# Kernel tuning notes

Measured on AMD Instinct MI355X. Metric: run time of the kernel, lower is better.

The kernel has to match this reference:

```python
import jax, jax.numpy as jnp
import numpy as np

D = 512      # input_size
BR = 4       # branching factor (fan-in per internal node)
DEPTH = 8    # leaf level index; levels 0..DEPTH, root at level 0
N_NODES = (BR ** (DEPTH + 1) - 1) // (BR - 1)  # 87381


def setup_inputs() -> dict:
    key = jax.random.key(0)
    k1, k2, k3 = jax.random.split(key, 3)
    vectors = jax.random.normal(k1, (N_NODES, D), dtype=jnp.float32)
    scale = 1.0 / np.sqrt(D)
    wl = jax.random.normal(k2, (D, D), dtype=jnp.float32) * scale
    wr = jax.random.normal(k3, (D, D), dtype=jnp.float32) * scale
    return {"vectors": vectors, "wl": wl, "wr": wr, "branching": BR, "depth": DEPTH}


def reference(vectors, wl, wr, branching, depth):
    """Levelized CBTree forward over a complete `branching`-ary tree.

    vectors: [N, D] BFS-ordered node vectors (level l starts at (B^l-1)/(B-1)).
    Per node: h = tanh(x + sum_i lc_i * (h_i @ wl.T) + rc_i * (h_i @ wr.T)).
    """
    B, L = int(branching), int(depth)
    d = vectors.shape[-1]
    if B > 1:
        ind = jnp.arange(1, B + 1, dtype=vectors.dtype)  # 1-based child index
        lc = (B - ind) / (B - 1)
        rc = (ind - 1) / (B - 1)
    else:
        lc = jnp.full((1,), 0.5, dtype=vectors.dtype)
        rc = lc
    offsets = [(B ** l - 1) // (B - 1) for l in range(L + 1)]
    # leaves contribute their raw vectors (child.vector, no transform at leaf)
    h = vectors[offsets[L]: offsets[L] + B ** L]
    for l in range(L - 1, -1, -1):
        n = B ** l
        x = vectors[offsets[l]: offsets[l] + n]          # [n, D]
        hc = h.reshape(n, B, d)                           # children of level l
        tl = jnp.einsum('nbd,ed->nbe', hc, wl)            # wl(h_i) (Linear: h @ W.T)
        tr = jnp.einsum('nbd,ed->nbe', hc, wr)
        agg = jnp.einsum('b,nbe->ne', lc, tl) + jnp.einsum('b,nbe->ne', rc, tr)
        h = jnp.tanh(x + agg)                             # [n, D]
    return h  # [1, D] root hidden state
```

## Files before the change

kernel.cpp:

```cpp
#include <hip/hip_runtime.h>

typedef short short8 __attribute__((ext_vector_type(8)));
typedef float f32x4 __attribute__((ext_vector_type(4)));

#define D 512
#define KDIM 1024

static __device__ __forceinline__ unsigned short f2b(float f) {
    unsigned u = __builtin_bit_cast(unsigned, f);
    unsigned r = (u + 0x7fffu + ((u >> 16) & 1u)) >> 16;
    return (unsigned short)r;
}
static __device__ __forceinline__ float b2f(unsigned short u) {
    return __builtin_bit_cast(float, ((unsigned)u) << 16);
}
static __device__ __forceinline__ void split(float v, unsigned short& hi, unsigned short& lo) {
    hi = f2b(v);
    lo = f2b(v - b2f(hi));
}

static __device__ __forceinline__ void g2lds(const void* g, void* l) {
    __builtin_amdgcn_global_load_lds(
        (const __attribute__((address_space(1))) unsigned int*)g,
        (__attribute__((address_space(3))) unsigned int*)l, 16, 0, 0);
}

__global__ void pre_kernel(const float* __restrict__ leaves,
                           const float* __restrict__ wl, const float* __restrict__ wr,
                           unsigned short* __restrict__ Ah7,
                           unsigned short* __restrict__ Wh, unsigned short* __restrict__ Wl,
                           unsigned short* __restrict__ zbase) {
    int b = blockIdx.x;
    if (b < 4096) {
        int t = b * 256 + threadIdx.x;
        int p = t >> 6;
        int kc = (t & 63) << 3;
        const float c13 = 1.0f / 3.0f, c23 = 2.0f / 3.0f;
        const float* child = leaves;
        float4 a0 = *reinterpret_cast<const float4*>(child + (size_t)(4 * p + 0) * D + kc);
        float4 a1 = *reinterpret_cast<const float4*>(child + (size_t)(4 * p + 0) * D + kc + 4);
        float4 b0 = *reinterpret_cast<const float4*>(child + (size_t)(4 * p + 1) * D + kc);
        float4 b1 = *reinterpret_cast<const float4*>(child + (size_t)(4 * p + 1) * D + kc + 4);
        float4 c0 = *reinterpret_cast<const float4*>(child + (size_t)(4 * p + 2) * D + kc);
        float4 c1 = *reinterpret_cast<const float4*>(child + (size_t)(4 * p + 2) * D + kc + 4);
        float4 d0 = *reinterpret_cast<const float4*>(child + (size_t)(4 * p + 3) * D + kc);
        float4 d1 = *reinterpret_cast<const float4*>(child + (size_t)(4 * p + 3) * D + kc + 4);
        float ca[8] = {a0.x, a0.y, a0.z, a0.w, a1.x, a1.y, a1.z, a1.w};
        float cb[8] = {b0.x, b0.y, b0.z, b0.w, b1.x, b1.y, b1.z, b1.w};
        float cc[8] = {c0.x, c0.y, c0.z, c0.w, c1.x, c1.y, c1.z, c1.w};
        float cd[8] = {d0.x, d0.y, d0.z, d0.w, d1.x, d1.y, d1.z, d1.w};
        short8 uh, vh;
#pragma unroll
        for (int j = 0; j < 8; ++j) {
            float u = ca[j] + c23 * cb[j] + c13 * cc[j];
            float v = c13 * cb[j] + c23 * cc[j] + cd[j];
            uh[j] = (short)f2b(u);
            vh[j] = (short)f2b(v);
        }
        *reinterpret_cast<short8*>(&Ah7[(size_t)p * KDIM + kc]) = uh;
        *reinterpret_cast<short8*>(&Ah7[(size_t)p * KDIM + 512 + kc]) = vh;
    } else if (b < 6144) {
        int t = (b - 4096) * 256 + threadIdx.x;
        int e = t >> 10, k = t & 1023;
        float v = (k < 512) ? wl[e * 512 + k] : wr[e * 512 + (k - 512)];
        unsigned short h, l;
        split(v, h, l);
        Wh[t] = h; Wl[t] = l;
    } else {
        int t = (b - 6144) * 256 + threadIdx.x;
        *reinterpret_cast<short8*>(zbase + (size_t)t * 8) = (short8)0;
    }
}

template <int BM, bool ALO, bool WLO>
__global__ __launch_bounds__(256)
void gemm_tanh(const unsigned short* __restrict__ Ah, const unsigned short* __restrict__ Al,
               const unsigned short* __restrict__ Wh, const unsigned short* __restrict__ Wl,
               const float* __restrict__ x,
               unsigned short* __restrict__ nAh, unsigned short* __restrict__ nAl,
               int n) {
    constexpr int MF = (BM == 128) ? 4 : 2;
    constexpr int NF = 4;
    constexpr int APASS = BM / 32;
    __shared__ __align__(16) unsigned short Ahs[BM][64];
    __shared__ __align__(16) unsigned short Als[ALO ? BM : 1][64];
    __shared__ __align__(16) unsigned short Bhs[128][64];
    __shared__ __align__(16) unsigned short Bls[WLO ? 128 : 1][64];
    const int m0 = blockIdx.x * BM;
    const int e0 = blockIdx.y * 128;
    const int tid = threadIdx.x;
    const int lane = tid & 63, wid = tid >> 6;
    const int wr = (wid >> 1) * (BM / 2);
    const int wc = (wid & 1) * 64;

    f32x4 acc[MF][NF];
#pragma unroll
    for (int m = 0; m < MF; ++m)
#pragma unroll
        for (int nn = 0; nn < NF; ++nn) acc[m][nn] = (f32x4){0.f, 0.f, 0.f, 0.f};

    const int lrow = lane >> 3;
    const int lcol = (lane & 7) << 3;

    for (int kb = 0; kb < KDIM; kb += 64) {
#pragma unroll
        for (int p = 0; p < APASS; ++p) {
            int row = p * 32 + wid * 8;
            size_t g = (size_t)(m0 + row + lrow) * KDIM + kb + lcol;
            g2lds(&Ah[g], &Ahs[row][0]);
            if (ALO) g2lds(&Al[g], &Als[ALO ? row : 0][0]);
        }
#pragma unroll
        for (int p = 0; p < 4; ++p) {
            int row = p * 32 + wid * 8;
            size_t g = (size_t)(e0 + row + lrow) * KDIM + kb + lcol;
            g2lds(&Wh[g], &Bhs[row][0]);
            if (WLO) g2lds(&Wl[g], &Bls[WLO ? row : 0][0]);
        }
        __syncthreads();
#pragma unroll
        for (int kk = 0; kk < 64; kk += 32) {
            const int ka = kk + ((lane >> 4) << 3);
            short8 afh[MF], afl[MF], bfh[NF], bfl[NF];
#pragma unroll
            for (int m = 0; m < MF; ++m) {
                afh[m] = *reinterpret_cast<const short8*>(&Ahs[wr + m * 16 + (lane & 15)][ka]);
                if (ALO) afl[m] = *reinterpret_cast<const short8*>(&Als[ALO ? (wr + m * 16 + (lane & 15)) : 0][ka]);
            }
#pragma unroll
            for (int nn = 0; nn < NF; ++nn) {
                bfh[nn] = *reinterpret_cast<const short8*>(&Bhs[wc + nn * 16 + (lane & 15)][ka]);
                if (WLO) bfl[nn] = *reinterpret_cast<const short8*>(&Bls[WLO ? (wc + nn * 16 + (lane & 15)) : 0][ka]);
            }
#pragma unroll
            for (int m = 0; m < MF; ++m)
#pragma unroll
                for (int nn = 0; nn < NF; ++nn) {
                    acc[m][nn] = __builtin_amdgcn_mfma_f32_16x16x32_bf16(afh[m], bfh[nn], acc[m][nn], 0, 0, 0);
                    if (WLO)
                        acc[m][nn] = __builtin_amdgcn_mfma_f32_16x16x32_bf16(afh[m], bfl[nn], acc[m][nn], 0, 0, 0);
                    if (ALO)
                        acc[m][nn] = __builtin_amdgcn_mfma_f32_16x16x32_bf16(afl[m], bfh[nn], acc[m][nn], 0, 0, 0);
                }
        }
        __syncthreads();
    }

    const int dr = (lane >> 4) << 2;
    const int dc = lane & 15;
    const float c13 = 1.0f / 3.0f, c23 = 2.0f / 3.0f;
#pragma unroll
    for (int m = 0; m < MF; ++m) {
        int rbase = m0 + wr + m * 16 + dr;
        if (rbase >= n) continue;
#pragma unroll
        for (int nn = 0; nn < NF; ++nn) {
            int col = e0 + wc + nn * 16 + dc;
            float hv[4];
#pragma unroll
            for (int j = 0; j < 4; ++j) {
                int row = rbase + j;
                hv[j] = (row < n) ? tanhf(acc[m][nn][j] + x[(size_t)row * D + col]) : 0.f;
            }
            int p = rbase >> 2;
            float u = hv[0] + c23 * hv[1] + c13 * hv[2];
            float v = c13 * hv[1] + c23 * hv[2] + hv[3];
            unsigned short h_, l_;
            split(u, h_, l_);
            nAh[(size_t)p * KDIM + col] = h_;
            nAl[(size_t)p * KDIM + col] = l_;
            split(v, h_, l_);
            nAh[(size_t)p * KDIM + 512 + col] = h_;
            nAl[(size_t)p * KDIM + 512 + col] = l_;
        }
    }
}

#define TBUF 6
template <bool FINAL>
__global__ __launch_bounds__(256)
void gemm_tiny(const unsigned short* __restrict__ Ah, const unsigned short* __restrict__ Al,
               const unsigned short* __restrict__ Wh, const unsigned short* __restrict__ Wl,
               const float* __restrict__ x,
               unsigned short* __restrict__ nAh, unsigned short* __restrict__ nAl,
               float* __restrict__ out, int n) {
    __shared__ __align__(16) unsigned short AhS[TBUF][32][64];
    __shared__ __align__(16) unsigned short AlS[TBUF][32][64];
    __shared__ __align__(16) unsigned short BhS[TBUF][64][64];
    __shared__ __align__(16) unsigned short BlS[TBUF][64][64];
    const int m0 = blockIdx.x * 32;
    const int e0 = blockIdx.y * 64;
    const int tid = threadIdx.x;
    const int lane = tid & 63, wid = tid >> 6;
    const int lrow = lane >> 3, lcol = (lane & 7) << 3;

    auto stage = [&](int s) {
        int slot = s % TBUF;
        int kb = s * 64;
        {
            int row = wid * 8;
            size_t g = (size_t)(m0 + row + lrow) * KDIM + kb + lcol;
            g2lds(&Ah[g], &AhS[slot][row][0]);
            g2lds(&Al[g], &AlS[slot][row][0]);
        }
#pragma unroll
        for (int p = 0; p < 2; ++p) {
            int row = wid * 16 + p * 8;
            size_t g = (size_t)(e0 + row + lrow) * KDIM + kb + lcol;
            g2lds(&Wh[g], &BhS[slot][row][0]);
            g2lds(&Wl[g], &BlS[slot][row][0]);
        }
    };

    f32x4 acc[2];
    acc[0] = (f32x4){0.f, 0.f, 0.f, 0.f};
    acc[1] = (f32x4){0.f, 0.f, 0.f, 0.f};

    stage(0); stage(1); stage(2); stage(3); stage(4);

#pragma unroll
    for (int t = 0; t < 16; ++t) {
        if (t <= 11)      { asm volatile("s_waitcnt vmcnt(24)" ::: "memory"); }
        else if (t == 12) { asm volatile("s_waitcnt vmcnt(18)" ::: "memory"); }
        else if (t == 13) { asm volatile("s_waitcnt vmcnt(12)" ::: "memory"); }
        else if (t == 14) { asm volatile("s_waitcnt vmcnt(6)"  ::: "memory"); }
        else              { asm volatile("s_waitcnt vmcnt(0)"  ::: "memory"); }
        __builtin_amdgcn_sched_barrier(0);
        __builtin_amdgcn_s_barrier();
        __builtin_amdgcn_sched_barrier(0);
        if (t + 5 < 16) stage(t + 5);
        const int slot = t % TBUF;
#pragma unroll
        for (int kk = 0; kk < 64; kk += 32) {
            const int ka = kk + ((lane >> 4) << 3);
            short8 afh[2], afl[2], bh, bl;
#pragma unroll
            for (int m = 0; m < 2; ++m) {
                afh[m] = *reinterpret_cast<const short8*>(&AhS[slot][m * 16 + (lane & 15)][ka]);
                afl[m] = *reinterpret_cast<const short8*>(&AlS[slot][m * 16 + (lane & 15)][ka]);
            }
            bh = *reinterpret_cast<const short8*>(&BhS[slot][wid * 16 + (lane & 15)][ka]);
            bl = *reinterpret_cast<const short8*>(&BlS[slot][wid * 16 + (lane & 15)][ka]);
#pragma unroll
            for (int m = 0; m < 2; ++m) {
                acc[m] = __builtin_amdgcn_mfma_f32_16x16x32_bf16(afh[m], bh, acc[m], 0, 0, 0);
                acc[m] = __builtin_amdgcn_mfma_f32_16x16x32_bf16(afh[m], bl, acc[m], 0, 0, 0);
                acc[m] = __builtin_amdgcn_mfma_f32_16x16x32_bf16(afl[m], bh, acc[m], 0, 0, 0);
            }
        }
    }

    const int dr = (lane >> 4) << 2;
    const int dc = lane & 15;
    const float c13 = 1.0f / 3.0f, c23 = 2.0f / 3.0f;
#pragma unroll
    for (int m = 0; m < 2; ++m) {
        int rbase = m0 + m * 16 + dr;
        if (rbase >= n) continue;
        int col = e0 + wid * 16 + dc;
        float hv[4];
#pragma unroll
        for (int j = 0; j < 4; ++j) {
            int row = rbase + j;
            hv[j] = (row < n) ? tanhf(acc[m][j] + x[(size_t)row * D + col]) : 0.f;
        }
        if (FINAL) {
            if (rbase == 0) out[col] = hv[0];
        } else {
            int p = rbase >> 2;
            float u = hv[0] + c23 * hv[1] + c13 * hv[2];
            float v = c13 * hv[1] + c23 * hv[2] + hv[3];
            unsigned short h_, l_;
            split(u, h_, l_);
            nAh[(size_t)p * KDIM + col] = h_;
            nAl[(size_t)p * KDIM + col] = l_;
            split(v, h_, l_);
            nAh[(size_t)p * KDIM + 512 + col] = h_;
            nAl[(size_t)p * KDIM + 512 + col] = l_;
        }
    }
}

extern "C" void kernel_launch(void* const* d_in, const int* in_sizes, int n_in,
                              void* d_out, int out_size, void* d_ws, size_t ws_size,
                              hipStream_t stream) {
    const float* vectors = (const float*)d_in[0];
    const float* wl = (const float*)d_in[1];
    const float* wr = (const float*)d_in[2];
    float* out = (float*)d_out;
    char* ws = (char*)d_ws;

    size_t cur = 0;
    auto alloc = [&](size_t bytes) -> char* {
        char* p = ws + cur;
        cur += (bytes + 255) & ~(size_t)255;
        return p;
    };
    unsigned short* Wh = (unsigned short*)alloc((size_t)512 * 1024 * 2);
    unsigned short* Wl = (unsigned short*)alloc((size_t)512 * 1024 * 2);
    const int arows[8] = {32, 32, 32, 64, 256, 1024, 4096, 16384};
    unsigned short *Ah[8], *Al[8];
    for (int l = 7; l >= 0; --l) {
        Ah[l] = (unsigned short*)alloc((size_t)arows[l] * KDIM * 2);
        Al[l] = (unsigned short*)alloc((size_t)arows[l] * KDIM * 2);
    }

    size_t off8 = 0;
    { size_t o = 0, c = 1; for (int l = 0; l <= 8; ++l) { if (l == 8) off8 = o; o += c; c *= 4; } }
    size_t off7 = off8 - 16384;

    pre_kernel<<<6240, 256, 0, stream>>>(vectors + off8 * (size_t)D, wl, wr,
                                         Ah[7], Wh, Wl, Ah[2]);

    gemm_tanh<128, false, false><<<dim3(128, 4), 256, 0, stream>>>(
        Ah[7], nullptr, Wh, nullptr, vectors + off7 * (size_t)D, Ah[6], Al[6], 16384);

    gemm_tanh<64, true, true><<<dim3(64, 4), 256, 0, stream>>>(
        Ah[6], Al[6], Wh, Wl, vectors + (off7 - 4096) * (size_t)D, Ah[5], Al[5], 4096);

    const int xo[6] = {0, 1, 5, 21, 85, 341};
    for (int l = 5; l >= 1; --l) {
        int n = 1 << (2 * l);
        int gx = (n + 31) / 32;
        gemm_tiny<false><<<dim3(gx, 8), 256, 0, stream>>>(
            Ah[l], Al[l], Wh, Wl, vectors + (size_t)xo[l] * D,
            Ah[l - 1], Al[l - 1], nullptr, n);
    }
    gemm_tiny<true><<<dim3(1, 8), 256, 0, stream>>>(
        Ah[0], Al[0], Wh, Wl, vectors, nullptr, nullptr, out, 1);
}
```

Measured before the change: 202.8 us.

## Fuse small tree levels into one cooperative kernel with grid syncs

The six small levels (5 down to root), previously launched as separate gemm_tiny kernels, now run in a single cooperative kernel. It loops over levels, strides tiles across 128 blocks and separates levels with grid.sync(), which removes several kernel launch gaps. The first two big GEMMs also stop writing the unused low-half (Al) output for level 6, since level 6 no longer reads Al. The cost is grid-barrier latency, less per-level parallelism when one level has more than 128 tiles, and an extra __syncthreads per tile. A fallback to the old per-level launches runs if the cooperative launch fails.

Result: slower. 298.0 us (+46.9%).

```diff
diff --git a/kernel.cpp b/kernel.cpp
--- a/kernel.cpp
+++ b/kernel.cpp
@@ -1,4 +1,7 @@
 #include <hip/hip_runtime.h>
+#include <hip/hip_cooperative_groups.h>
+
+namespace cg = cooperative_groups;
 
 typedef short short8 __attribute__((ext_vector_type(8)));
 typedef float f32x4 __attribute__((ext_vector_type(4)));
@@ -72,7 +75,7 @@
     }
 }
 
-template <int BM, bool ALO, bool WLO>
+template <int BM, bool ALO, bool WLO, bool WRL>
 __global__ __launch_bounds__(256)
 void gemm_tanh(const unsigned short* __restrict__ Ah, const unsigned short* __restrict__ Al,
                const unsigned short* __restrict__ Wh, const unsigned short* __restrict__ Wl,
@@ -168,28 +171,23 @@
             unsigned short h_, l_;
             split(u, h_, l_);
             nAh[(size_t)p * KDIM + col] = h_;
-            nAl[(size_t)p * KDIM + col] = l_;
+            if (WRL) nAl[(size_t)p * KDIM + col] = l_;
             split(v, h_, l_);
             nAh[(size_t)p * KDIM + 512 + col] = h_;
-            nAl[(size_t)p * KDIM + 512 + col] = l_;
+            if (WRL) nAl[(size_t)p * KDIM + 512 + col] = l_;
         }
     }
 }
 
 #define TBUF 6
-template <bool FINAL>
-__global__ __launch_bounds__(256)
-void gemm_tiny(const unsigned short* __restrict__ Ah, const unsigned short* __restrict__ Al,
-               const unsigned short* __restrict__ Wh, const unsigned short* __restrict__ Wl,
-               const float* __restrict__ x,
-               unsigned short* __restrict__ nAh, unsigned short* __restrict__ nAl,
-               float* __restrict__ out, int n) {
-    __shared__ __align__(16) unsigned short AhS[TBUF][32][64];
-    __shared__ __align__(16) unsigned short AlS[TBUF][32][64];
-    __shared__ __align__(16) unsigned short BhS[TBUF][64][64];
-    __shared__ __align__(16) unsigned short BlS[TBUF][64][64];
-    const int m0 = blockIdx.x * 32;
-    const int e0 = blockIdx.y * 64;
+static __device__ __forceinline__ void tiny_tile(
+    const unsigned short* __restrict__ Ah, const unsigned short* __restrict__ Al,
+    const unsigned short* __restrict__ Wh, const unsigned short* __restrict__ Wl,
+    const float* __restrict__ x,
+    unsigned short* __restrict__ nAh, unsigned short* __restrict__ nAl,
+    float* __restrict__ out, int n, int m0, int e0, bool finalLevel,
+    unsigned short (&AhS)[TBUF][32][64], unsigned short (&AlS)[TBUF][32][64],
+    unsigned short (&BhS)[TBUF][64][64], unsigned short (&BlS)[TBUF][64][64]) {
     const int tid = threadIdx.x;
     const int lane = tid & 63, wid = tid >> 6;
     const int lrow = lane >> 3, lcol = (lane & 7) << 3;
@@ -250,6 +248,8 @@
         }
     }
 
+    __syncthreads();
+
     const int dr = (lane >> 4) << 2;
     const int dc = lane & 15;
     const float c13 = 1.0f / 3.0f, c23 = 2.0f / 3.0f;
@@ -264,7 +264,7 @@
             int row = rbase + j;
             hv[j] = (row < n) ? tanhf(acc[m][j] + x[(size_t)row * D + col]) : 0.f;
         }
-        if (FINAL) {
+        if (finalLevel) {
             if (rbase == 0) out[col] = hv[0];
         } else {
             int p = rbase >> 2;
@@ -278,6 +278,58 @@
             nAh[(size_t)p * KDIM + 512 + col] = h_;
             nAl[(size_t)p * KDIM + 512 + col] = l_;
         }
+    }
+}
+
+template <bool FINAL>
+__global__ __launch_bounds__(256)
+void gemm_tiny_k(const unsigned short* __restrict__ Ah, const unsigned short* __restrict__ Al,
+                 const unsigned short* __restrict__ Wh, const unsigned short* __restrict__ Wl,
+                 const float* __restrict__ x,
+                 unsigned short* __restrict__ nAh, unsigned short* __restrict__ nAl,
+                 float* __restrict__ out, int n) {
+    __shared__ __align__(16) unsigned short AhS[TBUF][32][64];
+    __shared__ __align__(16) unsigned short AlS[TBUF][32][64];
+    __shared__ __align__(16) unsigned short BhS[TBUF][64][64];
+    __shared__ __align__(16) unsigned short BlS[TBUF][64][64];
+    tiny_tile(Ah, Al, Wh, Wl, x, nAh, nAl, out, n,
+              blockIdx.x * 32, blockIdx.y * 64, FINAL, AhS, AlS, BhS, BlS);
+}
+
+struct TailArgs {
+    const unsigned short* Wh;
+    const unsigned short* Wl;
+    unsigned short* Ah[6];
+    unsigned short* Al[6];
+    const float* vectors;
+    float* out;
+};
+
+__global__ __launch_bounds__(256)
+void coop_tail(TailArgs a) {
+    __shared__ __align__(16) unsigned short AhS[TBUF][32][64];
+    __shared__ __align__(16) unsigned short AlS[TBUF][32][64];
+    __shared__ __align__(16) unsigned short BhS[TBUF][64][64];
+    __shared__ __align__(16) unsigned short BlS[TBUF][64][64];
+    cg::grid_group grid = cg::this_grid();
+
+    for (int l = 5; l >= 0; --l) {
+        int n = 1 << (2 * l);
+        int gx = (n + 31) >> 5;
+        int tiles = gx * 8;
+        for (int t = (int)blockIdx.x; t < tiles; t += (int)gridDim.x) {
+            int m0 = (t >> 3) * 32;
+            int e0 = (t & 7) * 64;
+            int xo = ((1 << (2 * l)) - 1) / 3;
+            tiny_tile(a.Ah[l], a.Al[l], a.Wh, a.Wl,
+                      a.vectors + (size_t)xo * D,
+                      (l > 0) ? a.Ah[l - 1] : nullptr,
+                      (l > 0) ? a.Al[l - 1] : nullptr,
+                      (l == 0) ? a.out : nullptr,
+                      n, m0, e0, (l == 0),
+                      AhS, AlS, BhS, BlS);
+        }
+        if (l > 0) grid.sync();
     }
 }
 
@@ -312,20 +364,29 @@
     pre_kernel<<<6240, 256, 0, stream>>>(vectors + off8 * (size_t)D, wl, wr,
                                          Ah[7], Wh, Wl, Ah[2]);
 
-    gemm_tanh<128, false, false><<<dim3(128, 4), 256, 0, stream>>>(
-        Ah[7], nullptr, Wh, nullptr, vectors + off7 * (size_t)D, Ah[6], Al[6], 16384);
-
-    gemm_tanh<64, true, true><<<dim3(64, 4), 256, 0, stream>>>(
-        Ah[6], Al[6], Wh, Wl, vectors + (off7 - 4096) * (size_t)D, Ah[5], Al[5], 4096);
-
-    const int xo[6] = {0, 1, 5, 21, 85, 341};
-    for (int l = 5; l >= 1; --l) {
-        int n = 1 << (2 * l);
-        int gx = (n + 31) / 32;
-        gemm_tiny<false><<<dim3(gx, 8), 256, 0, stream>>>(
-            Ah[l], Al[l], Wh, Wl, vectors + (size_t)xo[l] * D,
-            Ah[l - 1], Al[l - 1], nullptr, n);
-    }
-    gemm_tiny<true><<<dim3(1, 8), 256, 0, stream>>>(
-        Ah[0], Al[0], Wh, Wl, vectors, nullptr, nullptr, out, 1);
-}
+    gemm_tanh<128, false, false, false><<<dim3(128, 4), 256, 0, stream>>>(
+        Ah[7], nullptr, Wh, nullptr, vectors + off7 * (size_t)D, Ah[6], nullptr, 16384);
+
+    gemm_tanh<64, false, true, true><<<dim3(64, 4), 256, 0, stream>>>(
+        Ah[6], nullptr, Wh, Wl, vectors + (off7 - 4096) * (size_t)D, Ah[5], Al[5], 4096);
+
+    TailArgs ta;
+    ta.Wh = Wh; ta.Wl = Wl;
+    for (int l = 0; l < 6; ++l) { ta.Ah[l] = Ah[l]; ta.Al[l] = Al[l]; }
+    ta.vectors = vectors;
+    ta.out = out;
+    void* kp[] = { &ta };
+    hipError_t cerr = hipLaunchCooperativeKernel((void*)coop_tail, dim3(128), dim3(256), kp, 0, stream);
+    if (cerr != hipSuccess) {
+        const int xo[6] = {0, 1, 5, 21, 85, 341};
+        for (int l = 5; l >= 1; --l) {
+            int n = 1 << (2 * l);
+            int gx = (n + 31) / 32;
+            gemm_tiny_k<false><<<dim3(gx, 8), 256, 0, stream>>>(
+                Ah[l], Al[l], Wh, Wl, vectors + (size_t)xo[l] * D,
+                Ah[l - 1], Al[l - 1], nullptr, n);
+        }
+        gemm_tiny_k<true><<<dim3(1, 8), 256, 0, stream>>>(
+            Ah[0], Al[0], Wh, Wl, vectors, nullptr, nullptr, out, 1);
+    }
+}
```
